# Optimization experiments

Measured on AMD Instinct MI355X. Metric: run time of the kernel, lower is better.

## Reference

```python
import jax, jax.numpy as jnp
import numpy as np

B, T = 64, 4096
ATTN_RNN_DIM, HYPERNET_DIM = 1024, 256
CHANNELS, KERNEL_SIZE, OUT_DIM = 32, 31, 128
PAD = (KERNEL_SIZE - 1) // 2


def setup_inputs() -> dict:
    key = jax.random.key(0)
    ks = jax.random.split(key, 8)
    s = 0.02
    return {
        "query": jax.random.normal(ks[0], (B, ATTN_RNN_DIM), jnp.float32),
        "prev_attn": jax.random.uniform(ks[1], (B, T), jnp.float32),
        "W1": jax.random.normal(ks[2], (HYPERNET_DIM, ATTN_RNN_DIM), jnp.float32) * s,
        "b1": jnp.zeros((HYPERNET_DIM,), jnp.float32),
        "W2": jax.random.normal(ks[3], (CHANNELS * KERNEL_SIZE, HYPERNET_DIM), jnp.float32) * s,
        "b2": jnp.zeros((CHANNELS * KERNEL_SIZE,), jnp.float32),
        "Wfc": jax.random.normal(ks[4], (OUT_DIM, CHANNELS), jnp.float32) * s,
        "bfc": jnp.zeros((OUT_DIM,), jnp.float32),
    }


def reference(query, prev_attn, W1, b1, W2, b2, Wfc, bfc):
    # hypernet: Linear -> tanh -> Linear, producing per-sample conv weights
    h = jnp.tanh(query @ W1.T + b1)                       # [B, hypernet_dim]
    convweight = (h @ W2.T + b2).reshape(B, CHANNELS, KERNEL_SIZE)  # [B, C, K]

    # per-sample depthwise conv1d (cross-correlation, 'same' padding)
    padded = jnp.pad(prev_attn, ((0, 0), (PAD, PAD)))     # [B, T+K-1]
    idx = jnp.arange(KERNEL_SIZE)[:, None] + jnp.arange(T)[None, :]  # [K, T]
    windows = padded[:, idx]                              # [B, K, T]
    x = jnp.einsum('bck,bkt->btc', convweight, windows)   # [B, T, C]

    # output linear
    return x @ Wfc.T + bfc                                # [B, T, out_dim]
```

## Files before the change

### kernel.cpp

```cpp
#include <hip/hip_runtime.h>

#define B 64
#define T 4096
#define AD 1024
#define HD 256
#define CH 32
#define KS 31
#define OD 128
#define PADW 15
#define CWN (CH*KS)
#define TILE_T 64
#define NTILE (T / TILE_T)
#define PADROW 128

__global__ __launch_bounds__(256) void k_hyper1(const float* __restrict__ q,
        const float* __restrict__ W1, const float* __restrict__ b1,
        float* __restrict__ h) {
    int wid  = blockIdx.x * 4 + (threadIdx.x >> 6);
    int lane = threadIdx.x & 63;
    int b = wid >> 8;
    int j = wid & 255;
    const float4* qr = (const float4*)(q  + (size_t)b * AD);
    const float4* wr = (const float4*)(W1 + (size_t)j * AD);
    float s = 0.f;
    #pragma unroll
    for (int m = 0; m < 4; ++m) {
        float4 a = qr[m * 64 + lane];
        float4 w = wr[m * 64 + lane];
        s += a.x * w.x + a.y * w.y + a.z * w.z + a.w * w.w;
    }
    #pragma unroll
    for (int off = 32; off > 0; off >>= 1)
        s += __shfl_down(s, off, 64);
    if (lane == 0) h[b * HD + j] = tanhf(s + b1[j]);
}

__global__ __launch_bounds__(256) void k_cw(const float* __restrict__ h,
        const float* __restrict__ W2, const float* __restrict__ b2,
        float* __restrict__ cw) {
    int b   = blockIdx.x >> 2;
    int qtr = blockIdx.x & 3;
    int tid = threadIdx.x;
    __shared__ float hs[HD];
    hs[tid] = h[(size_t)b * HD + tid];
    __syncthreads();
    int r = qtr * 248 + tid;
    if (tid < 248) {
        const float4* wr = (const float4*)(W2 + (size_t)r * HD);
        float s = 0.f;
        #pragma unroll
        for (int m = 0; m < HD / 4; ++m) {
            float4 w = wr[m];
            s += w.x * hs[4*m+0] + w.y * hs[4*m+1]
               + w.z * hs[4*m+2] + w.w * hs[4*m+3];
        }
        cw[(size_t)b * CWN + r] = s + b2[r];
    }
}

__global__ __launch_bounds__(256) void k_G(const float* __restrict__ cw,
        const float* __restrict__ Wfc, float* __restrict__ Gt) {
    int b   = blockIdx.x >> 2;
    int qtr = blockIdx.x & 3;
    int tid = threadIdx.x;
    __shared__ float cws[CWN];
    __shared__ float wfs_t[CH * OD];
    #pragma unroll
    for (int p = 0; p < 4; ++p) {
        int idx = p * 256 + tid;
        if (idx < CWN) cws[idx] = cw[(size_t)b * CWN + idx];
    }
    #pragma unroll
    for (int p = 0; p < 16; ++p) {
        int idx = p * 256 + tid;
        int o = idx >> 5, c = idx & 31;
        wfs_t[c * OD + o] = Wfc[idx];
    }
    __syncthreads();
    if (tid < 248) {
        int base = qtr * 992 + tid * 4;
        #pragma unroll
        for (int j = 0; j < 4; ++j) {
            int idx = base + j;
            int k = idx >> 7, o = idx & 127;
            float s = 0.f;
            #pragma unroll
            for (int c = 0; c < CH; ++c)
                s += wfs_t[c * OD + o] * cws[c * KS + k];
            Gt[(size_t)b * (KS * OD) + idx] = s;
        }
    }
}

__device__ __forceinline__ void compute_chunk(const float* pa, int s0, float base,
                                              const float (&g)[KS], float (&acc)[8]) {
    float pw[40];
    const float4* lp = (const float4*)(pa + s0);
    #pragma unroll
    for (int q4 = 0; q4 < 10; ++q4) {
        float4 v = lp[q4];
        pw[q4*4+0] = v.x; pw[q4*4+1] = v.y; pw[q4*4+2] = v.z; pw[q4*4+3] = v.w;
    }
    #pragma unroll
    for (int tt = 0; tt < 8; ++tt) {
        float a = base;
        #pragma unroll
        for (int k = 0; k < KS; ++k)
            a += g[k] * pw[tt + k];
        acc[tt] = a;
    }
}

__global__ __launch_bounds__(256, 4) void k_conv(const float* __restrict__ pa_g,
        const float* __restrict__ Gt, const float* __restrict__ bfc,
        float* __restrict__ out) {
    int bid  = blockIdx.x;
    int sid  = (bid & 7) * 512 + (bid >> 3);
    int b    = sid >> 6;
    int tile = sid & 63;
    int t0   = tile * TILE_T;
    int tid  = threadIdx.x;
    __shared__ float tileo[TILE_T][PADROW];
    __shared__ float pa[TILE_T + 32];

    if (tid < TILE_T + 32) {
        int gg = t0 + tid - PADW;
        pa[tid] = (gg >= 0 && gg < T) ? pa_g[(size_t)b * T + gg] : 0.f;
    }
    int o = tid & 127, half = tid >> 7;
    float g[KS];
    #pragma unroll
    for (int k = 0; k < KS; ++k)
        g[k] = Gt[(size_t)b * (KS * OD) + k * OD + o];
    float base = bfc[o];
    size_t obase = ((size_t)b * T + t0) * OD;
    __syncthreads();

    #pragma unroll
    for (int c = 0; c < 4; ++c) {
        int s0 = half * 32 + c * 8;
        float acc[8];
        compute_chunk(pa, s0, base, g, acc);
        #pragma unroll
        for (int tt = 0; tt < 8; ++tt)
            tileo[s0 + tt][o] = acc[tt];
        __syncthreads();
        #pragma unroll
        for (int j = 0; j < 2; ++j) {
            int f  = j * 256 + tid;
            int rl = f >> 5, c4 = f & 31;
            int row = (j == 0) ? (c * 8 + rl) : (32 + c * 8 + (rl - 8));
            float4 v = *(const float4*)&tileo[row][c4 * 4];
            *(float4*)(out + obase + (size_t)row * OD + c4 * 4) = v;
        }
    }
}

extern "C" void kernel_launch(void* const* d_in, const int* in_sizes, int n_in,
                              void* d_out, int out_size, void* d_ws, size_t ws_size,
                              hipStream_t stream) {
    const float* query = (const float*)d_in[0];
    const float* prev  = (const float*)d_in[1];
    const float* W1    = (const float*)d_in[2];
    const float* b1    = (const float*)d_in[3];
    const float* W2    = (const float*)d_in[4];
    const float* b2    = (const float*)d_in[5];
    const float* Wfc   = (const float*)d_in[6];
    const float* bfc   = (const float*)d_in[7];
    float* out = (float*)d_out;

    float* h  = (float*)d_ws;
    float* cw = h + B * HD;
    float* Gt = cw + B * CWN;

    k_hyper1<<<dim3(4096), dim3(256), 0, stream>>>(query, W1, b1, h);
    k_cw    <<<dim3(B * 4), dim3(256), 0, stream>>>(h, W2, b2, cw);
    k_G     <<<dim3(B * 4), dim3(256), 0, stream>>>(cw, Wfc, Gt);
    k_conv  <<<dim3(B * NTILE), dim3(256), 0, stream>>>(prev, Gt, bfc, out);
}
```

Before: 55.37 us.

## Restructure conv kernel to 4-channel x 8-row register tiles with direct float4 stores

The conv kernel now stages the per-batch G matrix in shared memory and has each thread compute a 4-output-channel by 8-timestep register tile. Results go straight to global memory as float4 stores, which removes the shared output tile and the per-chunk barriers. Occupancy hint is raised from 4 to 5 blocks. The cost is loading the full G matrix into LDS per block and doing 31 float4 LDS reads per thread, and each row is now written by 32 threads in one 512B contiguous segment.

```diff
diff --git a/kernel.cpp b/kernel.cpp
--- a/kernel.cpp
+++ b/kernel.cpp
@@ -11,7 +11,6 @@
 #define CWN (CH*KS)
 #define TILE_T 64
 #define NTILE (T / TILE_T)
-#define PADROW 128
 
 __global__ __launch_bounds__(256) void k_hyper1(const float* __restrict__ q,
         const float* __restrict__ W1, const float* __restrict__ b1,
@@ -92,26 +91,7 @@
     }
 }
 
-__device__ __forceinline__ void compute_chunk(const float* pa, int s0, float base,
-                                              const float (&g)[KS], float (&acc)[8]) {
-    float pw[40];
-    const float4* lp = (const float4*)(pa + s0);
-    #pragma unroll
-    for (int q4 = 0; q4 < 10; ++q4) {
-        float4 v = lp[q4];
-        pw[q4*4+0] = v.x; pw[q4*4+1] = v.y; pw[q4*4+2] = v.z; pw[q4*4+3] = v.w;
-    }
-    #pragma unroll
-    for (int tt = 0; tt < 8; ++tt) {
-        float a = base;
-        #pragma unroll
-        for (int k = 0; k < KS; ++k)
-            a += g[k] * pw[tt + k];
-        acc[tt] = a;
-    }
-}
-
-__global__ __launch_bounds__(256, 4) void k_conv(const float* __restrict__ pa_g,
+__global__ __launch_bounds__(256, 5) void k_conv(const float* __restrict__ pa_g,
         const float* __restrict__ Gt, const float* __restrict__ bfc,
         float* __restrict__ out) {
     int bid  = blockIdx.x;
@@ -120,40 +100,52 @@
     int tile = sid & 63;
     int t0   = tile * TILE_T;
     int tid  = threadIdx.x;
-    __shared__ float tileo[TILE_T][PADROW];
+    __shared__ float Gl[KS * OD];
     __shared__ float pa[TILE_T + 32];
 
-    if (tid < TILE_T + 32) {
+    #pragma unroll
+    for (int p = 0; p < 16; ++p) {
+        int idx = p * 256 + tid;
+        if (idx < KS * OD) Gl[idx] = Gt[(size_t)b * (KS * OD) + idx];
+    }
+    if (tid < TILE_T + 30) {
         int gg = t0 + tid - PADW;
         pa[tid] = (gg >= 0 && gg < T) ? pa_g[(size_t)b * T + gg] : 0.f;
     }
-    int o = tid & 127, half = tid >> 7;
-    float g[KS];
-    #pragma unroll
-    for (int k = 0; k < KS; ++k)
-        g[k] = Gt[(size_t)b * (KS * OD) + k * OD + o];
-    float base = bfc[o];
-    size_t obase = ((size_t)b * T + t0) * OD;
     __syncthreads();
 
+    int o4 = (tid & 31) * 4;
+    int s0 = (tid >> 5) * 8;
+    float4 base = *(const float4*)(bfc + o4);
+
+    float pw[40];
+    const float4* pv = (const float4*)(pa + s0);
     #pragma unroll
-    for (int c = 0; c < 4; ++c) {
-        int s0 = half * 32 + c * 8;
-        float acc[8];
-        compute_chunk(pa, s0, base, g, acc);
+    for (int q4 = 0; q4 < 10; ++q4) {
+        float4 v = pv[q4];
+        pw[q4*4+0] = v.x; pw[q4*4+1] = v.y; pw[q4*4+2] = v.z; pw[q4*4+3] = v.w;
+    }
+
+    float4 acc[8];
+    #pragma unroll
+    for (int r = 0; r < 8; ++r) acc[r] = base;
+    #pragma unroll
+    for (int k = 0; k < KS; ++k) {
+        float4 gk = *(const float4*)&Gl[k * OD + o4];
         #pragma unroll
-        for (int tt = 0; tt < 8; ++tt)
-            tileo[s0 + tt][o] = acc[tt];
-        __syncthreads();
-        #pragma unroll
-        for (int j = 0; j < 2; ++j) {
-            int f  = j * 256 + tid;
-            int rl = f >> 5, c4 = f & 31;
-            int row = (j == 0) ? (c * 8 + rl) : (32 + c * 8 + (rl - 8));
-            float4 v = *(const float4*)&tileo[row][c4 * 4];
-            *(float4*)(out + obase + (size_t)row * OD + c4 * 4) = v;
+        for (int r = 0; r < 8; ++r) {
+            float p = pw[r + k];
+            acc[r].x += gk.x * p;
+            acc[r].y += gk.y * p;
+            acc[r].z += gk.z * p;
+            acc[r].w += gk.w * p;
         }
     }
+
+    size_t obase = ((size_t)b * T + t0) * OD + o4;
+    #pragma unroll
+    for (int r = 0; r < 8; ++r)
+        *(float4*)(out + obase + (size_t)(s0 + r) * OD) = acc[r];
 }
 
 extern "C" void kernel_launch(void* const* d_in, const int* in_sizes, int n_in,
```

New measurement: 56.20 us. Within noise of the previous version (+1.5%).

## Fuse hypernet conv-weight and G kernels; double conv tile length per block

Applied to the files above, without the earlier changes.

Merges the k_cw and k_G kernels into a single k_cwG kernel. Each block computes the conv weights for one group of 8 taps across all channels, keeps them in shared memory and immediately produces the matching rows of G, so one launch and the global cw round-trip go away. The conv kernel now covers 128 timesteps per block in two passes, which halves the grid and the number of per-block G register loads. The cost is more serial work per block and fewer blocks to spread across CUs.

```diff
diff --git a/kernel.cpp b/kernel.cpp
--- a/kernel.cpp
+++ b/kernel.cpp
@@ -9,9 +9,8 @@
 #define OD 128
 #define PADW 15
 #define CWN (CH*KS)
-#define TILE_T 64
+#define TILE_T 128
 #define NTILE (T / TILE_T)
-#define PADROW 128
 
 __global__ __launch_bounds__(256) void k_hyper1(const float* __restrict__ q,
         const float* __restrict__ W1, const float* __restrict__ b1,
@@ -35,41 +34,16 @@
     if (lane == 0) h[b * HD + j] = tanhf(s + b1[j]);
 }
 
-__global__ __launch_bounds__(256) void k_cw(const float* __restrict__ h,
+__global__ __launch_bounds__(256) void k_cwG(const float* __restrict__ h,
         const float* __restrict__ W2, const float* __restrict__ b2,
-        float* __restrict__ cw) {
-    int b   = blockIdx.x >> 2;
-    int qtr = blockIdx.x & 3;
+        const float* __restrict__ Wfc, float* __restrict__ Gt) {
+    int b = blockIdx.x >> 2;
+    int q = blockIdx.x & 3;
     int tid = threadIdx.x;
     __shared__ float hs[HD];
+    __shared__ float cwl[CH * 8];
+    __shared__ float wfs_t[CH * OD];
     hs[tid] = h[(size_t)b * HD + tid];
-    __syncthreads();
-    int r = qtr * 248 + tid;
-    if (tid < 248) {
-        const float4* wr = (const float4*)(W2 + (size_t)r * HD);
-        float s = 0.f;
-        #pragma unroll
-        for (int m = 0; m < HD / 4; ++m) {
-            float4 w = wr[m];
-            s += w.x * hs[4*m+0] + w.y * hs[4*m+1]
-               + w.z * hs[4*m+2] + w.w * hs[4*m+3];
-        }
-        cw[(size_t)b * CWN + r] = s + b2[r];
-    }
-}
-
-__global__ __launch_bounds__(256) void k_G(const float* __restrict__ cw,
-        const float* __restrict__ Wfc, float* __restrict__ Gt) {
-    int b   = blockIdx.x >> 2;
-    int qtr = blockIdx.x & 3;
-    int tid = threadIdx.x;
-    __shared__ float cws[CWN];
-    __shared__ float wfs_t[CH * OD];
-    #pragma unroll
-    for (int p = 0; p < 4; ++p) {
-        int idx = p * 256 + tid;
-        if (idx < CWN) cws[idx] = cw[(size_t)b * CWN + idx];
-    }
     #pragma unroll
     for (int p = 0; p < 16; ++p) {
         int idx = p * 256 + tid;
@@ -77,17 +51,34 @@
         wfs_t[c * OD + o] = Wfc[idx];
     }
     __syncthreads();
-    if (tid < 248) {
-        int base = qtr * 992 + tid * 4;
-        #pragma unroll
-        for (int j = 0; j < 4; ++j) {
-            int idx = base + j;
-            int k = idx >> 7, o = idx & 127;
+    {
+        int c = tid >> 3, kk = tid & 7;
+        int k = q * 8 + kk;
+        if (k < KS) {
+            int r = c * KS + k;
+            const float4* wr  = (const float4*)(W2 + (size_t)r * HD);
+            const float4* hs4 = (const float4*)hs;
+            float s = 0.f;
+            #pragma unroll
+            for (int m = 0; m < HD / 4; ++m) {
+                float4 w = wr[m], hv = hs4[m];
+                s += w.x * hv.x + w.y * hv.y + w.z * hv.z + w.w * hv.w;
+            }
+            cwl[c * 8 + kk] = s + b2[r];
+        }
+    }
+    __syncthreads();
+    #pragma unroll
+    for (int p = 0; p < 4; ++p) {
+        int idx = p * 256 + tid;
+        int kl = idx >> 7, o = idx & 127;
+        int kg = q * 8 + kl;
+        if (kg < KS) {
             float s = 0.f;
             #pragma unroll
             for (int c = 0; c < CH; ++c)
-                s += wfs_t[c * OD + o] * cws[c * KS + k];
-            Gt[(size_t)b * (KS * OD) + idx] = s;
+                s += wfs_t[c * OD + o] * cwl[c * 8 + kl];
+            Gt[(size_t)b * (KS * OD) + kg * OD + o] = s;
         }
     }
 }
@@ -115,15 +106,15 @@
         const float* __restrict__ Gt, const float* __restrict__ bfc,
         float* __restrict__ out) {
     int bid  = blockIdx.x;
-    int sid  = (bid & 7) * 512 + (bid >> 3);
-    int b    = sid >> 6;
-    int tile = sid & 63;
+    int sid  = (bid & 7) * 256 + (bid >> 3);
+    int b    = sid >> 5;
+    int tile = sid & 31;
     int t0   = tile * TILE_T;
     int tid  = threadIdx.x;
-    __shared__ float tileo[TILE_T][PADROW];
+    __shared__ float tileo[64][128];
     __shared__ float pa[TILE_T + 32];
 
-    if (tid < TILE_T + 32) {
+    if (tid < TILE_T + 30) {
         int gg = t0 + tid - PADW;
         pa[tid] = (gg >= 0 && gg < T) ? pa_g[(size_t)b * T + gg] : 0.f;
     }
@@ -133,25 +124,29 @@
     for (int k = 0; k < KS; ++k)
         g[k] = Gt[(size_t)b * (KS * OD) + k * OD + o];
     float base = bfc[o];
-    size_t obase = ((size_t)b * T + t0) * OD;
     __syncthreads();
 
     #pragma unroll
-    for (int c = 0; c < 4; ++c) {
-        int s0 = half * 32 + c * 8;
-        float acc[8];
-        compute_chunk(pa, s0, base, g, acc);
+    for (int pass = 0; pass < 2; ++pass) {
+        const float* pap = pa + pass * 64;
+        size_t obase = ((size_t)b * T + t0 + pass * 64) * OD;
         #pragma unroll
-        for (int tt = 0; tt < 8; ++tt)
-            tileo[s0 + tt][o] = acc[tt];
-        __syncthreads();
-        #pragma unroll
-        for (int j = 0; j < 2; ++j) {
-            int f  = j * 256 + tid;
-            int rl = f >> 5, c4 = f & 31;
-            int row = (j == 0) ? (c * 8 + rl) : (32 + c * 8 + (rl - 8));
-            float4 v = *(const float4*)&tileo[row][c4 * 4];
-            *(float4*)(out + obase + (size_t)row * OD + c4 * 4) = v;
+        for (int c = 0; c < 4; ++c) {
+            int s0 = half * 32 + c * 8;
+            float acc[8];
+            compute_chunk(pap, s0, base, g, acc);
+            #pragma unroll
+            for (int tt = 0; tt < 8; ++tt)
+                tileo[s0 + tt][o] = acc[tt];
+            __syncthreads();
+            #pragma unroll
+            for (int j = 0; j < 2; ++j) {
+                int f  = j * 256 + tid;
+                int rl = f >> 5, c4 = f & 31;
+                int row = (j == 0) ? (c * 8 + rl) : (32 + c * 8 + (rl - 8));
+                float4 v = *(const float4*)&tileo[row][c4 * 4];
+                *(float4*)(out + obase + (size_t)row * OD + c4 * 4) = v;
+            }
         }
     }
 }
@@ -170,11 +165,9 @@
     float* out = (float*)d_out;
 
     float* h  = (float*)d_ws;
-    float* cw = h + B * HD;
-    float* Gt = cw + B * CWN;
+    float* Gt = h + B * HD;
 
     k_hyper1<<<dim3(4096), dim3(256), 0, stream>>>(query, W1, b1, h);
-    k_cw    <<<dim3(B * 4), dim3(256), 0, stream>>>(h, W2, b2, cw);
-    k_G     <<<dim3(B * 4), dim3(256), 0, stream>>>(cw, Wfc, Gt);
+    k_cwG   <<<dim3(B * 4), dim3(256), 0, stream>>>(h, W2, b2, Wfc, Gt);
     k_conv  <<<dim3(B * NTILE), dim3(256), 0, stream>>>(prev, Gt, bfc, out);
 }
```

Result: faster. 53.04 us (-4.2%).
